# Kernel optimization log

Measured on AMD Instinct MI355X. Metric: run time of the kernel, lower is better.

The kernel has to match this reference:

```python
import jax, jax.numpy as jnp
import numpy as np

B, D, L = 8, 512, 4096
NHEAD = 8
HEAD_DIM = D // NHEAD
TRUNC_STD = 0.02


def setup_inputs() -> dict:
    key = jax.random.key(0)
    ks = jax.random.split(key, 7)
    return {
        "x": jax.random.normal(ks[0], (B, D, L, 1), jnp.float32),
        "y": jax.random.normal(ks[1], (B, D, 1, 1), jnp.float32),
        "Wq": jax.random.normal(ks[2], (D, D), jnp.float32) * TRUNC_STD,
        "Wk": jax.random.normal(ks[3], (D, D), jnp.float32) * TRUNC_STD,
        "Wv": jax.random.normal(ks[4], (D, D), jnp.float32) * TRUNC_STD,
        "WO_ring": jax.random.normal(ks[5], (D, D), jnp.float32) * TRUNC_STD,
        "bO_ring": jnp.zeros((D,), jnp.float32),
        "WO_star": jax.random.normal(ks[6], (D, D), jnp.float32) * TRUNC_STD,
        "bO_star": jnp.zeros((D,), jnp.float32),
    }


def reference(x, y, Wq, Wk, Wv, WO_ring, bO_ring, WO_star, bO_star):
    Bx, Dx, Lx, _ = x.shape
    hd = Dx // NHEAD
    scale = 1.0 / np.sqrt(hd).astype(np.float32)

    # concat relay token on the sequence axis, project q/k/v over channels
    xy = jnp.concatenate([x, y], axis=2)[..., 0]            # [B, D, L+1]
    xy = jnp.transpose(xy, (0, 2, 1))                       # [B, L+1, D]
    q = jnp.transpose(xy @ Wq, (0, 2, 1))                   # [B, D, L+1]
    k = jnp.transpose(xy @ Wk, (0, 2, 1))
    v = jnp.transpose(xy @ Wv, (0, 2, 1))

    # ---- ring (local window-3 + relay) attention over the L node tokens ----
    qn = q[:, :, :Lx].reshape(Bx, NHEAD, hd, Lx)            # [B,n,h,L]
    kn, vn = k[:, :, :Lx], v[:, :, :Lx]                     # [B,D,L]
    kr, vr = k[:, :, Lx], v[:, :, Lx]                       # [B,D]

    def window3(t):
        # extract_patches SAME with size 3: slot w holds t[:, :, l-1+w], zero-padded
        tp = jnp.pad(t, ((0, 0), (0, 0), (1, 1)))
        tw = jnp.stack([tp[:, :, w:w + Lx] for w in range(3)], axis=2)  # [B,D,3,L]
        return tw.reshape(Bx, NHEAD, hd, 3, Lx)

    kr_b = jnp.broadcast_to(kr.reshape(Bx, NHEAD, hd, 1, 1), (Bx, NHEAD, hd, 1, Lx))
    vr_b = jnp.broadcast_to(vr.reshape(Bx, NHEAD, hd, 1, 1), (Bx, NHEAD, hd, 1, Lx))
    kw = jnp.concatenate([window3(kn), kr_b], axis=3)       # [B,n,h,4,L]
    vw = jnp.concatenate([window3(vn), vr_b], axis=3)

    scores = jnp.einsum('bnhl,bnhwl->bnwl', qn, kw) * scale  # [B,n,4,L]
    alphas = jax.nn.softmax(scores, axis=2)                  # softmax over window
    att = jnp.einsum('bnwl,bnhwl->bnhl', alphas, vw).reshape(Bx, Dx, Lx)
    nodes = jnp.einsum('bdl,de->bel', att, WO_ring) + bO_ring[None, :, None]
    nodes = nodes[..., None]                                 # [B, D, L, 1]

    # ---- star (relay) attention: relay query attends to all L+1 tokens ----
    qr = q[:, :, Lx].reshape(Bx, NHEAD, 1, hd)              # [B,n,1,h]
    ka = k.reshape(Bx, NHEAD, hd, Lx + 1)                   # [B,n,h,L+1]
    va = v.reshape(Bx, NHEAD, hd, Lx + 1)
    s = jnp.einsum('bnoh,bnhl->bnol', qr, ka) * scale       # [B,n,1,L+1]
    a = jax.nn.softmax(s, axis=-1)
    att_r = jnp.einsum('bnol,bnhl->bnoh', a, va).reshape(Bx, Dx)
    relay = (att_r @ WO_star + bO_star).reshape(Bx, Dx, 1, 1)

    return nodes, relay
```

## Files before the change

kernel.cpp:

```cpp
#include <hip/hip_runtime.h>

#define BB 8
#define DD 512
#define LL 4096
#define NH 8
#define HD 64
#define SCALE 0.125f
#define NCH2 128

typedef __attribute__((ext_vector_type(8))) short short8;
typedef __attribute__((ext_vector_type(4))) float f32x4;

static __device__ __forceinline__ float bf2f(unsigned short u) {
  union { float f; unsigned int i; } c; c.i = ((unsigned int)u) << 16; return c.f;
}
static __device__ __forceinline__ unsigned short f2bf(float f) {
  union { float f; unsigned int i; } c; c.f = f;
  unsigned int i = c.i;
  unsigned int r = (i + 0x7fffu + ((i >> 16) & 1u)) >> 16;
  return (unsigned short)r;
}

static __device__ __forceinline__ void gload_lds16(const void* g, void* l) {
  __builtin_amdgcn_global_load_lds(
      (const __attribute__((address_space(1))) void*)g,
      (__attribute__((address_space(3))) void*)l, 16, 0, 0);
}

static __device__ __forceinline__ float waveSum(float v) {
#pragma unroll
  for (int o = 32; o; o >>= 1) v += __shfl_down(v, o, 64);
  return v;
}
static __device__ __forceinline__ float grp8Sum(float v) {
  v += __shfl_xor(v, 1, 8);
  v += __shfl_xor(v, 2, 8);
  v += __shfl_xor(v, 4, 8);
  return v;
}
static __device__ __forceinline__ float waveAllMax(float v) {
#pragma unroll
  for (int o = 1; o < 64; o <<= 1) v = fmaxf(v, __shfl_xor(v, o, 64));
  return v;
}
static __device__ __forceinline__ float waveAllSum(float v) {
#pragma unroll
  for (int o = 1; o < 64; o <<= 1) v += __shfl_xor(v, o, 64);
  return v;
}

__global__ __launch_bounds__(256) void prep_all(
    const float* __restrict__ x, unsigned short* __restrict__ xt,
    const float* __restrict__ w0, const float* __restrict__ w1,
    const float* __restrict__ w2, const float* __restrict__ w3,
    unsigned short* __restrict__ o0, unsigned short* __restrict__ o1,
    unsigned short* __restrict__ o2, unsigned short* __restrict__ o3) {
  __shared__ float t[64][65];
  const int tid = threadIdx.x;
  const int r = tid >> 4;
  const int c4 = (tid & 15) * 4;
  if (blockIdx.z < BB) {
    const int b = blockIdx.z;
    const int e0 = blockIdx.y * 64;
    const int l0 = blockIdx.x * 64;
    const float* xb = x + (size_t)b * DD * LL;
#pragma unroll
    for (int p = 0; p < 4; p++) {
      const float4 v = *(const float4*)(xb + (size_t)(e0 + p * 16 + r) * LL + l0 + c4);
      *(float4*)&t[p * 16 + r][c4] = v;
    }
    __syncthreads();
#pragma unroll
    for (int p = 0; p < 4; p++) {
      const int ll = p * 16 + r;
      ushort4 o;
      o.x = f2bf(t[c4 + 0][ll]);
      o.y = f2bf(t[c4 + 1][ll]);
      o.z = f2bf(t[c4 + 2][ll]);
      o.w = f2bf(t[c4 + 3][ll]);
      *(ushort4*)(xt + ((size_t)b * LL + l0 + ll) * DD + e0 + c4) = o;
    }
  } else {
    const int wid = blockIdx.x + 64 * blockIdx.y;
    if (wid >= 256) return;
    const int s = wid >> 6;
    const int tb = wid & 63;
    const int m0 = (tb & 7) * 64;
    const int d0 = (tb >> 3) * 64;
    const float* win = (s == 0) ? w0 : (s == 1) ? w1 : (s == 2) ? w2 : w3;
    unsigned short* wout = (s == 0) ? o0 : (s == 1) ? o1 : (s == 2) ? o2 : o3;
#pragma unroll
    for (int p = 0; p < 4; p++) {
      const float4 v = *(const float4*)(win + (size_t)(d0 + p * 16 + r) * DD + m0 + c4);
      *(float4*)&t[p * 16 + r][c4] = v;
    }
    __syncthreads();
#pragma unroll
    for (int p = 0; p < 4; p++) {
      const int ll = p * 16 + r;
      ushort4 o;
      o.x = f2bf(t[c4 + 0][ll]);
      o.y = f2bf(t[c4 + 1][ll]);
      o.z = f2bf(t[c4 + 2][ll]);
      o.w = f2bf(t[c4 + 3][ll]);
      *(ushort4*)(wout + (size_t)(m0 + ll) * DD + d0 + c4) = o;
    }
  }
}

#define STAGEH(g, s)                                       \
  do {                                                     \
    gload_lds16((g) + sgoff, (s) + sloff);                 \
    gload_lds16((g) + sgoff + 32, (s) + sloff + 4096);     \
  } while (0)

#define READ_A(dst, base, ib)                                           \
  _Pragma("unroll") for (int i = 0; i < 4; i++) {                       \
    dst[i][0] = *(const short8*)((base) + ((ib) + i) * 512);            \
    dst[i][1] = *(const short8*)((base) + ((ib) + i) * 512 + 4096);     \
  }

#define READ_B(base, qn_)                                               \
  _Pragma("unroll") for (int j = 0; j < 2; j++) {                       \
    bb[j][0] = *(const short8*)((base) + (qn_) * 1024 + j * 512);       \
    bb[j][1] = *(const short8*)((base) + (qn_) * 1024 + j * 512 + 4096);\
  }

#define MFMA16(AF, IO, JO)                                                    \
  __builtin_amdgcn_s_setprio(1);                                              \
  _Pragma("unroll") for (int i = 0; i < 4; i++)                               \
  _Pragma("unroll") for (int j = 0; j < 2; j++) {                             \
    acc[(IO) + i][(JO) + j] = __builtin_amdgcn_mfma_f32_16x16x32_bf16(        \
        AF[i][0], bb[j][0], acc[(IO) + i][(JO) + j], 0, 0, 0);                \
    acc[(IO) + i][(JO) + j] = __builtin_amdgcn_mfma_f32_16x16x32_bf16(        \
        AF[i][1], bb[j][1], acc[(IO) + i][(JO) + j], 0, 0, 0);                \
  }                                                                           \
  __builtin_amdgcn_s_setprio(0);

#define PHASE_SYNC_PRE                                     \
  __builtin_amdgcn_s_barrier();                            \
  asm volatile("s_waitcnt lgkmcnt(0)" ::: "memory");       \
  __builtin_amdgcn_sched_barrier(0);

#define PHASE_SYNC_POST                                    \
  __builtin_amdgcn_sched_barrier(0);                       \
  __builtin_amdgcn_s_barrier();

#define GEMM_8PH_CORE                                                         \
  const int lane = tid & 63, w = tid >> 6;                                    \
  const int wm = w >> 2, wn = w & 3;                                          \
  const int l15 = lane & 15, lh = lane >> 4;                                  \
  const int kswz = (lh << 3) ^ ((l15 & 8) << 1);                              \
  const unsigned short* aB = sm + wm * 8192 + l15 * 32 + kswz;                \
  const unsigned short* bB = sm + 32768 + (wn >> 1) * 8192 +                  \
                             (wn & 1) * 2048 + l15 * 32 + kswz;               \
  const int srow = (w << 4) + (lane >> 2);                                    \
  const size_t sgoff = (size_t)srow * DD +                                    \
      ((size_t)(((lane & 3) << 3) ^ ((srow & 8) << 1)));                      \
  const int sloff = w * 512;                                                  \
  f32x4 acc[8][4];                                                            \
  _Pragma("unroll") for (int i = 0; i < 8; i++)                               \
  _Pragma("unroll") for (int j = 0; j < 4; j++)                               \
      acc[i][j] = (f32x4){0.f, 0.f, 0.f, 0.f};                                \
  STAGEH(Ag, sm);                                                             \
  STAGEH(Ag + 128 * DD, sm + 8192);                                           \
  STAGEH(Bg, sm + 32768);                                                     \
  STAGEH(Bg + 128 * DD, sm + 32768 + 8192);                                   \
  STAGEH(Ag + 64, sm + 16384);                                                \
  STAGEH(Ag + 128 * DD + 64, sm + 16384 + 8192);                              \
  asm volatile("s_waitcnt vmcnt(4)" ::: "memory");                            \
  __builtin_amdgcn_s_barrier();                                               \
  short8 a0[4][2], a1[4][2], bb[2][2];                                        \
  for (int u = 0; u < 8; ++u) {                                               \
    const int slot = u & 1;                                                   \
    const unsigned short* aS = aB + slot * 16384;                             \
    const unsigned short* bS = bB + slot * 16384;                             \
    const unsigned short* An = Ag + (u + 2) * 64;                             \
    const unsigned short* Bn = Bg + (u + 1) * 64;                             \
    unsigned short* sAd = sm + slot * 16384;                                  \
    unsigned short* sBd = sm + 32768 + (slot ^ 1) * 16384;                    \
    READ_A(a0, aS, 0);                                                        \
    READ_B(bS, 0);                                                            \
    if (u < 7) STAGEH(Bn, sBd);                                               \
    PHASE_SYNC_PRE                                                            \
    MFMA16(a0, 0, 0)                                                          \
    PHASE_SYNC_POST                                                           \
    READ_A(a1, aS, 4);                                                        \
    if (u < 7) STAGEH(Bn + 128 * DD, sBd + 8192);                             \
    PHASE_SYNC_PRE                                                            \
    MFMA16(a1, 4, 0)                                                          \
    PHASE_SYNC_POST                                                           \
    READ_B(bS, 1);                                                            \
    if (u < 6) STAGEH(An, sAd);                                               \
    PHASE_SYNC_PRE                                                            \
    MFMA16(a0, 0, 2)                                                          \
    PHASE_SYNC_POST                                                           \
    if (u < 6) STAGEH(An + 128 * DD, sAd + 8192);                             \
    __builtin_amdgcn_s_barrier();                                             \
    asm volatile("s_waitcnt lgkmcnt(0)" ::: "memory");                        \
    __builtin_amdgcn_sched_barrier(0);                                        \
    MFMA16(a1, 4, 2)                                                          \
    __builtin_amdgcn_sched_barrier(0);                                        \
    if (u < 6) {                                                              \
      asm volatile("s_waitcnt vmcnt(4)" ::: "memory");                        \
    } else if (u == 6) {                                                      \
      asm volatile("s_waitcnt vmcnt(0)" ::: "memory");                        \
    }                                                                         \
    __builtin_amdgcn_s_barrier();                                             \
  }

__global__ __launch_bounds__(512, 2) void qkv_mfma_8ph(
    const unsigned short* __restrict__ Wt, const unsigned short* __restrict__ Xt,
    unsigned short* __restrict__ qn, unsigned short* __restrict__ kn,
    unsigned short* __restrict__ vn) {
  extern __shared__ __align__(16) unsigned short sm[];
  const int b = blockIdx.z;
  const int m0 = blockIdx.y * 256;
  const int n0 = blockIdx.x * 256;
  const int tid = threadIdx.x;
  const unsigned short* Ag = Wt + (size_t)m0 * DD;
  const unsigned short* Bg = Xt + ((size_t)b * LL + n0) * DD;

  GEMM_8PH_CORE

  __syncthreads();
#pragma unroll
  for (int i = 0; i < 8; i++)
#pragma unroll
    for (int j = 0; j < 4; j++) {
      const int dloc = wm * 128 + i * 16 + lh * 4;
      const int lloc = wn * 64 + j * 16 + l15;
      ushort4 pk;
      pk.x = f2bf(acc[i][j][0]);
      pk.y = f2bf(acc[i][j][1]);
      pk.z = f2bf(acc[i][j][2]);
      pk.w = f2bf(acc[i][j][3]);
      *(ushort4*)((char*)sm + ((lloc * 512 + dloc * 2) ^ ((lloc & 7) << 4))) = pk;
    }
  __syncthreads();
  const int sector = m0 >> 9;
  unsigned short* outp = ((sector == 0) ? qn : (sector == 1) ? kn : vn) +
                         (size_t)b * LL * DD + (m0 & 511);
#pragma unroll
  for (int it = 0; it < 16; it++) {
    const int flat = it * 8192 + tid * 16;
    const int lloc = flat >> 9;
    const int off = flat & 511;
    const short8 vdat =
        *(const short8*)((const char*)sm + lloc * 512 + (off ^ ((lloc & 7) << 4)));
    *(short8*)(outp + (size_t)(n0 + lloc) * DD + (off >> 1)) = vdat;
  }
}

__global__ __launch_bounds__(512, 2) void nodes_mfma_8ph(
    const unsigned short* __restrict__ Wt, const unsigned short* __restrict__ At,
    const float* __restrict__ bo, float* __restrict__ out) {
  extern __shared__ __align__(16) unsigned short sm[];
  const int b = blockIdx.z;
  const int m0 = blockIdx.y * 256;
  const int n0 = blockIdx.x * 256;
  const int tid = threadIdx.x;
  const unsigned short* Ag = Wt + (size_t)m0 * DD;
  const unsigned short* Bg = At + ((size_t)b * LL + n0) * DD;

  GEMM_8PH_CORE

  float* outp = out + (size_t)b * DD * LL;
  const int ebase = m0 + wm * 128;
  const int col0 = n0 + wn * 64 + l15;
#pragma unroll
  for (int i = 0; i < 8; i++) {
    const int e0r = ebase + i * 16 + lh * 4;
#pragma unroll
    for (int r = 0; r < 4; r++) {
      const float bv = bo[e0r + r];
      float* rowp = outp + (size_t)(e0r + r) * LL + col0;
#pragma unroll
      for (int j = 0; j < 4; j++) rowp[j * 16] = acc[i][j][r] + bv;
    }
  }
}

__global__ __launch_bounds__(256) void relay_qkv(
    const float* __restrict__ y, const float* __restrict__ Wq,
    const float* __restrict__ Wk, const float* __restrict__ Wv,
    float* __restrict__ qr, float* __restrict__ kr, float* __restrict__ vr) {
  const int b = blockIdx.y;
  const int d0 = blockIdx.x * 64;
  const int tid = threadIdx.x;
  const int dl = tid & 63, eg = tid >> 6;
  __shared__ float ys[DD];
  __shared__ float r3[3][4][64];
  for (int i = tid; i < DD; i += 256) ys[i] = y[b * DD + i];
  __syncthreads();
  float aq = 0.f, ak = 0.f, av = 0.f;
  const int e0 = eg * 128;
  for (int e = e0; e < e0 + 128; e++) {
    const float yv = ys[e];
    aq = fmaf(yv, Wq[(size_t)e * DD + d0 + dl], aq);
    ak = fmaf(yv, Wk[(size_t)e * DD + d0 + dl], ak);
    av = fmaf(yv, Wv[(size_t)e * DD + d0 + dl], av);
  }
  r3[0][eg][dl] = aq;
  r3[1][eg][dl] = ak;
  r3[2][eg][dl] = av;
  __syncthreads();
  if (tid < 192) {
    const int m = tid >> 6, d = tid & 63;
    const float s = r3[m][0][d] + r3[m][1][d] + r3[m][2][d] + r3[m][3][d];
    float* dst = (m == 0) ? qr : (m == 1) ? kr : vr;
    dst[b * DD + d0 + d] = s;
  }
}

__global__ __launch_bounds__(256) void local_attn_f(
    const unsigned short* __restrict__ qn, const unsigned short* __restrict__ kn,
    const unsigned short* __restrict__ vn, const float* __restrict__ kr,
    const float* __restrict__ vr, const float* __restrict__ qrg,
    unsigned short* __restrict__ att_t, float* __restrict__ part) {
  const int b = blockIdx.z, n = blockIdx.y;
  const int tid = threadIdx.x;
  const int li = tid >> 3, dl = tid & 7;
  const int l0 = blockIdx.x * 32;
  const int l = l0 + li;
  __shared__ float krs[HD], vrs[HD], qrs[HD];
  __shared__ __align__(16) char ksb[34 * 128];
  __shared__ __align__(16) char vsb[34 * 128];
  __shared__ float sv2[32];
  __shared__ float os[32][68];
  const int rb = b * DD + n * HD;
  if (tid < HD) {
    krs[tid] = kr[rb + tid];
    vrs[tid] = vr[rb + tid];
    qrs[tid] = qrg[rb + tid];
  }

  {
    const int s1 = tid >> 3;
    const int gl1 = min(max(l0 - 1 + s1, 0), LL - 1);
    const size_t gb1 = ((size_t)b * LL + gl1) * DD + n * HD + dl * 8;
    const int so1 = s1 * 128 + dl * 16;
    *(short8*)(ksb + so1) = *(const short8*)(kn + gb1);
    *(short8*)(vsb + so1) = *(const short8*)(vn + gb1);
    if (tid < 16) {
      const int s2 = 32 + (tid >> 3);
      const int gl2 = min(l0 - 1 + s2, LL - 1);
      const size_t gb2 = ((size_t)b * LL + gl2) * DD + n * HD + dl * 8;
      const int so2 = s2 * 128 + dl * 16;
      *(short8*)(ksb + so2) = *(const short8*)(kn + gb2);
      *(short8*)(vsb + so2) = *(const short8*)(vn + gb2);
    }
  }
  __syncthreads();

  const size_t rowbase = ((size_t)b * LL + l) * DD + n * HD + dl * 8;
  const bool has_m = (l > 0), has_p = (l < LL - 1);
  const int lo = dl * 16;

  const short8 q8 = *(const short8*)(qn + rowbase);
  const short8 km8 = *(const short8*)(ksb + (li + 0) * 128 + lo);
  const short8 k08 = *(const short8*)(ksb + (li + 1) * 128 + lo);
  const short8 kp8 = *(const short8*)(ksb + (li + 2) * 128 + lo);

  float s0 = 0.f, s1 = 0.f, s2 = 0.f, s3 = 0.f;
  float qf[8];
#pragma unroll
  for (int j = 0; j < 8; j++) {
    qf[j] = bf2f((unsigned short)q8[j]);
    s0 = fmaf(qf[j], bf2f((unsigned short)km8[j]), s0);
    s1 = fmaf(qf[j], bf2f((unsigned short)k08[j]), s1);
    s2 = fmaf(qf[j], bf2f((unsigned short)kp8[j]), s2);
    s3 = fmaf(qf[j], krs[dl * 8 + j], s3);
  }
  s0 = grp8Sum(s0) * SCALE;
  s1 = grp8Sum(s1) * SCALE;
  s2 = grp8Sum(s2) * SCALE;
  s3 = grp8Sum(s3) * SCALE;
  if (!has_m) s0 = 0.f;
  if (!has_p) s2 = 0.f;
  const float m = fmaxf(fmaxf(s0, s1), fmaxf(s2, s3));
  const float e0 = __expf(s0 - m), e1 = __expf(s1 - m);
  const float e2 = __expf(s2 - m), e3 = __expf(s3 - m);
  const float inv = 1.f / (e0 + e1 + e2 + e3);
  const float a0 = has_m ? e0 * inv : 0.f;
  const float a1 = e1 * inv;
  const float a2 = has_p ? e2 * inv : 0.f;
  const float a3 = e3 * inv;

  const short8 vm8 = *(const short8*)(vsb + (li + 0) * 128 + lo);
  const short8 v08 = *(const short8*)(vsb + (li + 1) * 128 + lo);
  const short8 vp8 = *(const short8*)(vsb + (li + 2) * 128 + lo);
  short8 o8;
#pragma unroll
  for (int j = 0; j < 8; j++) {
    float o = a0 * bf2f((unsigned short)vm8[j]) + a1 * bf2f((unsigned short)v08[j]) +
              a2 * bf2f((unsigned short)vp8[j]) + a3 * vrs[dl * 8 + j];
    o8[j] = (short)f2bf(o);
  }
  *(short8*)(att_t + rowbase) = o8;

  {
    const short8 kc = *(const short8*)(ksb + (li + 1) * 128 + lo);
    float p = 0.f;
#pragma unroll
    for (int j = 0; j < 8; j++) p = fmaf(qrs[dl * 8 + j], bf2f((unsigned short)kc[j]), p);
    p = grp8Sum(p);
    if (dl == 0) sv2[li] = p * SCALE;
  }
  __syncthreads();
  const int lane = tid & 63;
  const float sval = sv2[lane & 31];
  const float m2 = waveAllMax(sval);
  const float sum2 = waveAllSum((lane < 32) ? __expf(sval - m2) : 0.f);
  const float pp = __expf(sv2[li] - m2);
  {
    const short8 vc = *(const short8*)(vsb + (li + 1) * 128 + lo);
#pragma unroll
    for (int j = 0; j < 8; j++) os[li][dl * 8 + j] = pp * bf2f((unsigned short)vc[j]);
  }
  __syncthreads();
  float* po = part + (((size_t)b * NH + n) * NCH2 + blockIdx.x) * 68;
  if (tid < HD) {
    float t = 0.f;
#pragma unroll 8
    for (int g = 0; g < 32; g++) t += os[g][tid];
    po[tid] = t;
  }
  if (tid == 64) { po[64] = m2; po[65] = sum2; }
}

__global__ __launch_bounds__(256) void relay_combine_par(
    const float* __restrict__ qr, const float* __restrict__ krr,
    const float* __restrict__ vrr, const float* __restrict__ part,
    float* __restrict__ attr) {
  const int n = blockIdx.x, b = blockIdx.y;
  const int tid = threadIdx.x;
  const int rb = b * DD + n * HD;
  __shared__ float lw[NCH2];
  __shared__ float red[8];
  __shared__ float o4[4][64];
  __shared__ float srs;
  const float* po = part + (((size_t)b * NH + n) * NCH2) * 68;

  float mloc = -1e30f;
  if (tid < NCH2) mloc = po[tid * 68 + 64];
  if (tid < 64) {
    float t = qr[rb + tid] * krr[rb + tid];
    t = waveAllSum(t);
    if (tid == 0) srs = t * SCALE;
  }
  const float wm_ = waveAllMax(mloc);
  if ((tid & 63) == 0) red[tid >> 6] = wm_;
  __syncthreads();
  const float M = fmaxf(fmaxf(fmaxf(red[0], red[1]), fmaxf(red[2], red[3])), srs);
  float spart = 0.f;
  if (tid < NCH2) {
    const float e = __expf(mloc - M);
    lw[tid] = e;
    spart = po[tid * 68 + 65] * e;
  }
  const float ws_ = waveAllSum(spart);
  if ((tid & 63) == 0) red[4 + (tid >> 6)] = ws_;
  __syncthreads();
  const float er = __expf(srs - M);
  const float S = er + red[4] + red[5] + red[6] + red[7];
  const int h = tid & 63, g = tid >> 6;
  float o = 0.f;
#pragma unroll 8
  for (int c = g * 32; c < g * 32 + 32; c++) o = fmaf(lw[c], po[c * 68 + h], o);
  o4[g][h] = o;
  __syncthreads();
  if (tid < 64) {
    const float oo =
        o4[0][tid] + o4[1][tid] + o4[2][tid] + o4[3][tid] + er * vrr[rb + tid];
    attr[rb + tid] = oo / S;
  }
}

__global__ __launch_bounds__(256) void relay_proj(
    const float* __restrict__ attr, const float* __restrict__ Wstar,
    const float* __restrict__ bstar, float* __restrict__ out) {
  const int b = blockIdx.y;
  const int e0 = blockIdx.x * 64;
  const int tid = threadIdx.x;
  const int el = tid & 63, dg = tid >> 6;
  __shared__ float as[DD];
  __shared__ float r[4][64];
  for (int i = tid; i < DD; i += 256) as[i] = attr[b * DD + i];
  __syncthreads();
  float acc = 0.f;
  const int d0 = dg * 128;
  for (int d = d0; d < d0 + 128; d++)
    acc = fmaf(as[d], Wstar[(size_t)d * DD + e0 + el], acc);
  r[dg][el] = acc;
  __syncthreads();
  if (tid < 64)
    out[(size_t)BB * DD * LL + b * DD + e0 + tid] =
        r[0][tid] + r[1][tid] + r[2][tid] + r[3][tid] + bstar[e0 + tid];
}

extern "C" void kernel_launch(void* const* d_in, const int* in_sizes, int n_in,
                              void* d_out, int out_size, void* d_ws, size_t ws_size,
                              hipStream_t stream) {
  const float* x   = (const float*)d_in[0];
  const float* y   = (const float*)d_in[1];
  const float* Wq  = (const float*)d_in[2];
  const float* Wk  = (const float*)d_in[3];
  const float* Wv  = (const float*)d_in[4];
  const float* WOr = (const float*)d_in[5];
  const float* bOr = (const float*)d_in[6];
  const float* WOs = (const float*)d_in[7];
  const float* bOs = (const float*)d_in[8];
  float* out = (float*)d_out;

  char* ws = (char*)d_ws;
  const size_t SZ = (size_t)BB * DD * LL * sizeof(unsigned short);
  unsigned short* qn  = (unsigned short*)(ws);
  unsigned short* kn  = (unsigned short*)(ws + SZ);
  unsigned short* vn  = (unsigned short*)(ws + 2 * SZ);
  unsigned short* xt  = (unsigned short*)(ws + 3 * SZ);
  unsigned short* att_t = xt;
  unsigned short* Wallt = (unsigned short*)(ws + 4 * SZ);
  unsigned short* WOrt  = (unsigned short*)(ws + 4 * SZ + 1536 * 512 * 2);
  float* qr   = (float*)(ws + 4 * SZ + 2048 * 512 * 2);
  float* kr   = qr + BB * DD;
  float* vr   = kr + BB * DD;
  float* attr = vr + BB * DD;
  float* part = attr + BB * DD;

  static int smaxset = 0;
  if (!smaxset) {
    (void)hipFuncSetAttribute((const void*)qkv_mfma_8ph,
                              hipFuncAttributeMaxDynamicSharedMemorySize, 131072);
    (void)hipFuncSetAttribute((const void*)nodes_mfma_8ph,
                              hipFuncAttributeMaxDynamicSharedMemorySize, 131072);
    smaxset = 1;
  }

  prep_all<<<dim3(64, 8, BB + 1), 256, 0, stream>>>(
      x, xt, Wq, Wk, Wv, WOr,
      Wallt, Wallt + (size_t)512 * 512, Wallt + (size_t)1024 * 512, WOrt);

  qkv_mfma_8ph<<<dim3(16, 6, BB), 512, 131072, stream>>>(Wallt, xt, qn, kn, vn);
  relay_qkv<<<dim3(8, BB), 256, 0, stream>>>(y, Wq, Wk, Wv, qr, kr, vr);
  local_attn_f<<<dim3(LL / 32, NH, BB), 256, 0, stream>>>(qn, kn, vn, kr, vr, qr,
                                                          att_t, part);
  nodes_mfma_8ph<<<dim3(16, 2, BB), 512, 131072, stream>>>(WOrt, att_t, bOr, out);
  relay_combine_par<<<dim3(NH, BB), 256, 0, stream>>>(qr, kr, vr, part, attr);
  relay_proj<<<dim3(8, BB), 256, 0, stream>>>(attr, WOs, bOs, out);
}
```

Before: 264.1 us.

## Fuse relay QKV into prep, stage GEMM epilogue via LDS, widen relay proj

Folds the relay q/k/v projection into otherwise idle blocks of the prep kernel, removing one kernel launch. The nodes GEMM epilogue now stages accumulators through swizzled shared memory so each wave writes full contiguous 16-byte rows instead of scattered 4-byte stores. The relay projection also uses twice as many blocks, each with a shorter reduction, to spread its work across more CUs. The epilogue adds extra barriers and an LDS round trip.

```diff
diff --git a/kernel.cpp b/kernel.cpp
--- a/kernel.cpp
+++ b/kernel.cpp
@@ -54,8 +54,12 @@
     const float* __restrict__ w0, const float* __restrict__ w1,
     const float* __restrict__ w2, const float* __restrict__ w3,
     unsigned short* __restrict__ o0, unsigned short* __restrict__ o1,
-    unsigned short* __restrict__ o2, unsigned short* __restrict__ o3) {
+    unsigned short* __restrict__ o2, unsigned short* __restrict__ o3,
+    const float* __restrict__ y, float* __restrict__ qr,
+    float* __restrict__ kr, float* __restrict__ vr) {
   __shared__ float t[64][65];
+  __shared__ float ys[DD];
+  __shared__ float r3[3][4][64];
   const int tid = threadIdx.x;
   const int r = tid >> 4;
   const int c4 = (tid & 15) * 4;
@@ -82,28 +86,54 @@
     }
   } else {
     const int wid = blockIdx.x + 64 * blockIdx.y;
-    if (wid >= 256) return;
-    const int s = wid >> 6;
-    const int tb = wid & 63;
-    const int m0 = (tb & 7) * 64;
-    const int d0 = (tb >> 3) * 64;
-    const float* win = (s == 0) ? w0 : (s == 1) ? w1 : (s == 2) ? w2 : w3;
-    unsigned short* wout = (s == 0) ? o0 : (s == 1) ? o1 : (s == 2) ? o2 : o3;
-#pragma unroll
-    for (int p = 0; p < 4; p++) {
-      const float4 v = *(const float4*)(win + (size_t)(d0 + p * 16 + r) * DD + m0 + c4);
-      *(float4*)&t[p * 16 + r][c4] = v;
-    }
-    __syncthreads();
-#pragma unroll
-    for (int p = 0; p < 4; p++) {
-      const int ll = p * 16 + r;
-      ushort4 o;
-      o.x = f2bf(t[c4 + 0][ll]);
-      o.y = f2bf(t[c4 + 1][ll]);
-      o.z = f2bf(t[c4 + 2][ll]);
-      o.w = f2bf(t[c4 + 3][ll]);
-      *(ushort4*)(wout + (size_t)(m0 + ll) * DD + d0 + c4) = o;
+    if (wid < 256) {
+      const int s = wid >> 6;
+      const int tb = wid & 63;
+      const int m0 = (tb & 7) * 64;
+      const int d0 = (tb >> 3) * 64;
+      const float* win = (s == 0) ? w0 : (s == 1) ? w1 : (s == 2) ? w2 : w3;
+      unsigned short* wout = (s == 0) ? o0 : (s == 1) ? o1 : (s == 2) ? o2 : o3;
+#pragma unroll
+      for (int p = 0; p < 4; p++) {
+        const float4 v = *(const float4*)(win + (size_t)(d0 + p * 16 + r) * DD + m0 + c4);
+        *(float4*)&t[p * 16 + r][c4] = v;
+      }
+      __syncthreads();
+#pragma unroll
+      for (int p = 0; p < 4; p++) {
+        const int ll = p * 16 + r;
+        ushort4 o;
+        o.x = f2bf(t[c4 + 0][ll]);
+        o.y = f2bf(t[c4 + 1][ll]);
+        o.z = f2bf(t[c4 + 2][ll]);
+        o.w = f2bf(t[c4 + 3][ll]);
+        *(ushort4*)(wout + (size_t)(m0 + ll) * DD + d0 + c4) = o;
+      }
+    } else if (wid < 320) {
+      const int rbk = wid - 256;
+      const int b = rbk >> 3;
+      const int d0 = (rbk & 7) * 64;
+      const int dl = tid & 63, eg = tid >> 6;
+      for (int i = tid; i < DD; i += 256) ys[i] = y[b * DD + i];
+      __syncthreads();
+      float aq = 0.f, ak = 0.f, av = 0.f;
+      const int e0 = eg * 128;
+      for (int e = e0; e < e0 + 128; e++) {
+        const float yv = ys[e];
+        aq = fmaf(yv, w0[(size_t)e * DD + d0 + dl], aq);
+        ak = fmaf(yv, w1[(size_t)e * DD + d0 + dl], ak);
+        av = fmaf(yv, w2[(size_t)e * DD + d0 + dl], av);
+      }
+      r3[0][eg][dl] = aq;
+      r3[1][eg][dl] = ak;
+      r3[2][eg][dl] = av;
+      __syncthreads();
+      if (tid < 192) {
+        const int m = tid >> 6, d = tid & 63;
+        const float s = r3[m][0][d] + r3[m][1][d] + r3[m][2][d] + r3[m][3][d];
+        float* dst = (m == 0) ? qr : (m == 1) ? kr : vr;
+        dst[b * DD + d0 + d] = s;
+      }
     }
   }
 }
@@ -266,50 +296,37 @@
   GEMM_8PH_CORE
 
   float* outp = out + (size_t)b * DD * LL;
-  const int ebase = m0 + wm * 128;
-  const int col0 = n0 + wn * 64 + l15;
-#pragma unroll
-  for (int i = 0; i < 8; i++) {
-    const int e0r = ebase + i * 16 + lh * 4;
-#pragma unroll
-    for (int r = 0; r < 4; r++) {
-      const float bv = bo[e0r + r];
-      float* rowp = outp + (size_t)(e0r + r) * LL + col0;
-#pragma unroll
-      for (int j = 0; j < 4; j++) rowp[j * 16] = acc[i][j][r] + bv;
-    }
-  }
-}
-
-__global__ __launch_bounds__(256) void relay_qkv(
-    const float* __restrict__ y, const float* __restrict__ Wq,
-    const float* __restrict__ Wk, const float* __restrict__ Wv,
-    float* __restrict__ qr, float* __restrict__ kr, float* __restrict__ vr) {
-  const int b = blockIdx.y;
-  const int d0 = blockIdx.x * 64;
-  const int tid = threadIdx.x;
-  const int dl = tid & 63, eg = tid >> 6;
-  __shared__ float ys[DD];
-  __shared__ float r3[3][4][64];
-  for (int i = tid; i < DD; i += 256) ys[i] = y[b * DD + i];
-  __syncthreads();
-  float aq = 0.f, ak = 0.f, av = 0.f;
-  const int e0 = eg * 128;
-  for (int e = e0; e < e0 + 128; e++) {
-    const float yv = ys[e];
-    aq = fmaf(yv, Wq[(size_t)e * DD + d0 + dl], aq);
-    ak = fmaf(yv, Wk[(size_t)e * DD + d0 + dl], ak);
-    av = fmaf(yv, Wv[(size_t)e * DD + d0 + dl], av);
-  }
-  r3[0][eg][dl] = aq;
-  r3[1][eg][dl] = ak;
-  r3[2][eg][dl] = av;
-  __syncthreads();
-  if (tid < 192) {
-    const int m = tid >> 6, d = tid & 63;
-    const float s = r3[m][0][d] + r3[m][1][d] + r3[m][2][d] + r3[m][3][d];
-    float* dst = (m == 0) ? qr : (m == 1) ? kr : vr;
-    dst[b * DD + d0 + d] = s;
+  float* smf = (float*)sm;
+#pragma unroll
+  for (int p = 0; p < 2; p++) {
+    __syncthreads();
+    if (wm == p) {
+#pragma unroll
+      for (int i = 0; i < 8; i++)
+#pragma unroll
+        for (int j = 0; j < 4; j++) {
+          const int lloc = wn * 64 + j * 16 + l15;
+#pragma unroll
+          for (int r = 0; r < 4; r++) {
+            const int er = i * 16 + lh * 4 + r;
+            *(float*)((char*)smf + ((er * 1024 + lloc * 4) ^ ((er & 7) << 4))) =
+                acc[i][j][r];
+          }
+        }
+    }
+    __syncthreads();
+#pragma unroll
+    for (int it = 0; it < 16; it++) {
+      const int row = it * 8 + w;
+      const f32x4 vv = *(const f32x4*)((const char*)smf +
+          ((row * 1024 + lane * 16) ^ ((row & 7) << 4)));
+      const int e = m0 + p * 128 + row;
+      const float bv = bo[e];
+      f32x4 rr;
+      rr[0] = vv[0] + bv; rr[1] = vv[1] + bv;
+      rr[2] = vv[2] + bv; rr[3] = vv[3] + bv;
+      *(f32x4*)(outp + (size_t)e * LL + n0 + lane * 4) = rr;
+    }
   }
 }
 
@@ -481,22 +498,25 @@
     const float* __restrict__ attr, const float* __restrict__ Wstar,
     const float* __restrict__ bstar, float* __restrict__ out) {
   const int b = blockIdx.y;
-  const int e0 = blockIdx.x * 64;
+  const int e0 = blockIdx.x * 32;
   const int tid = threadIdx.x;
-  const int el = tid & 63, dg = tid >> 6;
+  const int el = tid & 31, dg = tid >> 5;
   __shared__ float as[DD];
-  __shared__ float r[4][64];
+  __shared__ float r[8][32];
   for (int i = tid; i < DD; i += 256) as[i] = attr[b * DD + i];
   __syncthreads();
   float acc = 0.f;
-  const int d0 = dg * 128;
-  for (int d = d0; d < d0 + 128; d++)
+  const int d0 = dg * 64;
+  for (int d = d0; d < d0 + 64; d++)
     acc = fmaf(as[d], Wstar[(size_t)d * DD + e0 + el], acc);
   r[dg][el] = acc;
   __syncthreads();
-  if (tid < 64)
-    out[(size_t)BB * DD * LL + b * DD + e0 + tid] =
-        r[0][tid] + r[1][tid] + r[2][tid] + r[3][tid] + bstar[e0 + tid];
+  if (tid < 32) {
+    float s = bstar[e0 + tid];
+#pragma unroll
+    for (int g = 0; g < 8; g++) s += r[g][tid];
+    out[(size_t)BB * DD * LL + b * DD + e0 + tid] = s;
+  }
 }
 
 extern "C" void kernel_launch(void* const* d_in, const int* in_sizes, int n_in,
@@ -539,13 +559,13 @@
 
   prep_all<<<dim3(64, 8, BB + 1), 256, 0, stream>>>(
       x, xt, Wq, Wk, Wv, WOr,
-      Wallt, Wallt + (size_t)512 * 512, Wallt + (size_t)1024 * 512, WOrt);
+      Wallt, Wallt + (size_t)512 * 512, Wallt + (size_t)1024 * 512, WOrt,
+      y, qr, kr, vr);
 
   qkv_mfma_8ph<<<dim3(16, 6, BB), 512, 131072, stream>>>(Wallt, xt, qn, kn, vn);
-  relay_qkv<<<dim3(8, BB), 256, 0, stream>>>(y, Wq, Wk, Wv, qr, kr, vr);
   local_attn_f<<<dim3(LL / 32, NH, BB), 256, 0, stream>>>(qn, kn, vn, kr, vr, qr,
                                                           att_t, part);
   nodes_mfma_8ph<<<dim3(16, 2, BB), 512, 131072, stream>>>(WOrt, att_t, bOr, out);
   relay_combine_par<<<dim3(NH, BB), 256, 0, stream>>>(qr, kr, vr, part, attr);
-  relay_proj<<<dim3(8, BB), 256, 0, stream>>>(attr, WOs, bOs, out);
-}
+  relay_proj<<<dim3(16, BB), 256, 0, stream>>>(attr, WOs, bOs, out);
+}
```

New measurement: 277.0 us. +4.9%, slower.
